# Performance work log

Measured on AMD Instinct MI355X. Metric: run time of the kernel, lower is better.

## Reference

```python
import jax, jax.numpy as jnp
import numpy as np

K = 3
PAD = 1
DIL = 1
BN_EPS = 1e-5


def _unfold(x, k, pad, dil):
    # torch F.unfold with stride=1: (bs, c, h, w) -> (bs, c*k*k, h*w), c slowest.
    bs, c, h, w = x.shape
    xp = jnp.pad(x, ((0, 0), (0, 0), (pad, pad), (pad, pad)))
    cols = [xp[:, :, i * dil:i * dil + h, j * dil:j * dil + w]
            for i in range(k) for j in range(k)]
    return jnp.stack(cols, axis=2).reshape(bs, c * k * k, h * w)


def setup_inputs() -> dict:
    key = jax.random.key(0)
    ks = jax.random.split(key, 4)
    bs, c, h, w = 8, 3, 512, 512
    kk = K * K
    kernel = jax.random.normal(ks[0], (bs, kk, h, w), jnp.float32)
    inp = jax.random.normal(ks[1], (bs, c, h, w), jnp.float32)
    inp0 = jax.random.normal(ks[2], (bs, c, h, w), jnp.float32)
    conv_w = jax.random.normal(ks[3], (kk, kk * 3, 3, 3), jnp.float32) * 0.05
    return {
        "kernel": kernel,
        "input": inp,
        "input0": inp0,
        "conv_w": conv_w,
        "bn_gamma": jnp.ones((kk,), jnp.float32),
        "bn_beta": jnp.zeros((kk,), jnp.float32),
        "bn_mean": jnp.zeros((kk,), jnp.float32),
        "bn_var": jnp.ones((kk,), jnp.float32),
    }


def reference(kernel, input, input0, conv_w, bn_gamma, bn_beta, bn_mean, bn_var):
    bs, c, h, w = input.shape
    kk = K * K
    mid = (kk - 1) // 2  # 4 for K=3
    # im2col: (bs, c*k*k, h*w) = (bs, 27, hw)
    im = _unfold(input, K, PAD, DIL)
    # overwrite 3 center rows with input0
    im = im.at[:, mid:mid + 3, :].set(input0.reshape(bs, c, h * w))
    x = im.reshape(bs, c * kk, h, w)
    # 3x3 conv, 27 -> 9 channels, pad 1, no bias
    y = jax.lax.conv_general_dilated(
        x, conv_w, window_strides=(1, 1), padding=[(1, 1), (1, 1)],
        dimension_numbers=("NCHW", "OIHW", "NCHW"))
    # BatchNorm (inference: running stats)
    scale = (bn_gamma / jnp.sqrt(bn_var + BN_EPS))[None, :, None, None]
    shift = (bn_beta - bn_mean * bn_gamma / jnp.sqrt(bn_var + BN_EPS))[None, :, None, None]
    y = y * scale + shift
    # elementwise weighted reduce over the k*k axis
    out = jnp.einsum("bkp,bkp->bp", y.reshape(bs, kk, h * w),
                     kernel.reshape(bs, kk, h * w))
    return out.reshape(bs, 1, h, w)
```

## Files before the change

### kernel.cpp

```cpp
#include <hip/hip_runtime.h>

#define HW 512
#define CH 3
#define KK 9
#define BS 8
#define TW 32
#define TH 8


__global__ __launch_bounds__(256) void prep_kernel(
    const float* __restrict__ conv_w, const float* __restrict__ gamma,
    const float* __restrict__ beta, const float* __restrict__ mean,
    const float* __restrict__ var, float* __restrict__ ws) {
  const int tid = threadIdx.x;
  for (int t = tid; t < 675; t += 256) {
    int o = t % 9, tap = t / 9;
    int c = tap / 25, r = tap % 25, ey = r / 5, ex = r % 5;
    float s = gamma[o] * rsqrtf(var[o] + 1e-5f);
    float sum = 0.f;
    for (int dy = 0; dy < 3; ++dy) {
      int oy = ey - dy; if (oy < 0 || oy > 2) continue;
      for (int dx = 0; dx < 3; ++dx) {
        int ox = ex - dx; if (ox < 0 || ox > 2) continue;
        int off = oy * 3 + ox;
        if (c == 0 && off >= 4 && off <= 6) continue;
        sum += conv_w[((o * 27 + c * 9 + off) * 3 + dy) * 3 + dx];
      }
    }
    ws[t] = s * sum;
  }
  for (int t = tid; t < 243; t += 256) {
    int o = t % 9, tap = t / 9;
    int c = tap / 9, r = tap % 9, dy = r / 3, dx = r % 3;
    float s = gamma[o] * rsqrtf(var[o] + 1e-5f);
    ws[675 + t] = s * conv_w[((o * 27 + 4 + c) * 3 + dy) * 3 + dx];
  }
  for (int o = tid; o < 9; o += 256) {
    float s = gamma[o] * rsqrtf(var[o] + 1e-5f);
    ws[918 + o] = beta[o] - mean[o] * s;
  }
  for (int t = tid; t < 2187; t += 256) {
    int o = t % 9, q = t / 9;
    int ic = q / 9, r = q % 9, dy = r / 3, dx = r % 3;
    float s = gamma[o] * rsqrtf(var[o] + 1e-5f);
    ws[927 + t] = s * conv_w[((o * 27 + ic) * 3 + dy) * 3 + dx];
  }
}

__global__ __launch_bounds__(256) void main_kernel(
    const float* __restrict__ kern, const float* __restrict__ input,
    const float* __restrict__ input0, const float* __restrict__ ws,
    float* __restrict__ out) {
  __shared__ float in_t[3][TH + 4][TW + 4];
  __shared__ float in0_t[3][TH + 2][TW + 2];
  const int tid = threadIdx.x;
  const int b = blockIdx.z;
  const int x0 = blockIdx.x * TW, y0 = blockIdx.y * TH;
  const float* inp_b = input + (long)b * CH * HW * HW;
  const float* inp0_b = input0 + (long)b * CH * HW * HW;

  float* lin = &in_t[0][0][0];
  for (int i = tid; i < 3 * (TH + 4) * (TW + 4); i += 256) {
    int c = i / ((TH + 4) * (TW + 4));
    int r = i % ((TH + 4) * (TW + 4));
    int ry = r / (TW + 4), rx = r % (TW + 4);
    int gy = y0 + ry - 2, gx = x0 + rx - 2;
    float v = 0.f;
    if ((unsigned)gy < HW && (unsigned)gx < HW) v = inp_b[(c * HW + gy) * HW + gx];
    lin[i] = v;
  }
  float* lin0 = &in0_t[0][0][0];
  for (int i = tid; i < 3 * (TH + 2) * (TW + 2); i += 256) {
    int c = i / ((TH + 2) * (TW + 2));
    int r = i % ((TH + 2) * (TW + 2));
    int ry = r / (TW + 2), rx = r % (TW + 2);
    int gy = y0 + ry - 1, gx = x0 + rx - 1;
    float v = 0.f;
    if ((unsigned)gy < HW && (unsigned)gx < HW) v = inp0_b[(c * HW + gy) * HW + gx];
    lin0[i] = v;
  }
  __syncthreads();

  const int tx = tid & 31, ty = tid >> 5;
  const int X = x0 + tx, Y = y0 + ty;
  float acc[9];
#pragma unroll
  for (int o = 0; o < 9; ++o) acc[o] = 0.f;

#pragma unroll
  for (int c = 0; c < 3; ++c)
#pragma unroll
    for (int ey = 0; ey < 5; ++ey)
#pragma unroll
      for (int ex = 0; ex < 5; ++ex) {
        float v = in_t[c][ty + ey][tx + ex];
        const float* w = ws + (c * 25 + ey * 5 + ex) * 9;
#pragma unroll
        for (int o = 0; o < 9; ++o) acc[o] = fmaf(w[o], v, acc[o]);
      }

#pragma unroll
  for (int c = 0; c < 3; ++c)
#pragma unroll
    for (int ey = 0; ey < 3; ++ey)
#pragma unroll
      for (int ex = 0; ex < 3; ++ex) {
        float v = in0_t[c][ty + ey][tx + ex];
        const float* w = ws + 675 + (c * 9 + ey * 3 + ex) * 9;
#pragma unroll
        for (int o = 0; o < 9; ++o) acc[o] = fmaf(w[o], v, acc[o]);
      }

  const float* kb = kern + (long)b * KK * (HW * HW) + Y * HW + X;
  float result = 0.f;
#pragma unroll
  for (int o = 0; o < 9; ++o)
    result = fmaf(kb[(long)o * (HW * HW)], acc[o] + ws[918 + o], result);
  out[((long)b * HW + Y) * HW + X] = result;
}

__global__ __launch_bounds__(256) void border_kernel(
    const float* __restrict__ kern, const float* __restrict__ input,
    const float* __restrict__ input0, const float* __restrict__ ws,
    float* __restrict__ out) {
  const int per_img = 4 * HW - 4;
  int idx = blockIdx.x * blockDim.x + threadIdx.x;
  if (idx >= BS * per_img) return;
  int b = idx / per_img, p = idx % per_img;
  int X, Y;
  if (p < HW) { Y = 0; X = p; }
  else if (p < 2 * HW) { Y = HW - 1; X = p - HW; }
  else if (p < 3 * HW - 2) { X = 0; Y = p - 2 * HW + 1; }
  else { X = HW - 1; Y = p - (3 * HW - 2) + 1; }

  const float* inp_b = input + (long)b * CH * HW * HW;
  const float* inp0_b = input0 + (long)b * CH * HW * HW;
  float acc[9];
#pragma unroll
  for (int o = 0; o < 9; ++o) acc[o] = 0.f;

  for (int dy = 0; dy < 3; ++dy) {
    int yy = Y + dy - 1;
    if ((unsigned)yy >= HW) continue;
    for (int dx = 0; dx < 3; ++dx) {
      int xx = X + dx - 1;
      if ((unsigned)xx >= HW) continue;
      for (int c = 0; c < 3; ++c)
        for (int oy = 0; oy < 3; ++oy) {
          int iy = yy + oy - 1;
          for (int ox = 0; ox < 3; ++ox) {
            int off = oy * 3 + ox;
            if (c == 0 && off >= 4 && off <= 6) continue;
            int ix = xx + ox - 1;
            float v = 0.f;
            if ((unsigned)iy < HW && (unsigned)ix < HW)
              v = inp_b[(c * HW + iy) * HW + ix];
            const float* w = ws + 927 + ((c * 9 + off) * 9 + dy * 3 + dx) * 9;
#pragma unroll
            for (int o = 0; o < 9; ++o) acc[o] = fmaf(w[o], v, acc[o]);
          }
        }
      for (int c = 0; c < 3; ++c) {
        float v = inp0_b[(c * HW + yy) * HW + xx];
        const float* w = ws + 675 + (c * 9 + dy * 3 + dx) * 9;
#pragma unroll
        for (int o = 0; o < 9; ++o) acc[o] = fmaf(w[o], v, acc[o]);
      }
    }
  }
  const float* kb = kern + (long)b * KK * (HW * HW) + Y * HW + X;
  float result = 0.f;
#pragma unroll
  for (int o = 0; o < 9; ++o)
    result = fmaf(kb[(long)o * (HW * HW)], acc[o] + ws[918 + o], result);
  out[((long)b * HW + Y) * HW + X] = result;
}

extern "C" void kernel_launch(void* const* d_in, const int* in_sizes, int n_in,
                              void* d_out, int out_size, void* d_ws, size_t ws_size,
                              hipStream_t stream) {
  const float* kern   = (const float*)d_in[0];
  const float* input  = (const float*)d_in[1];
  const float* input0 = (const float*)d_in[2];
  const float* conv_w = (const float*)d_in[3];
  const float* gamma  = (const float*)d_in[4];
  const float* beta   = (const float*)d_in[5];
  const float* mean   = (const float*)d_in[6];
  const float* var    = (const float*)d_in[7];
  float* out = (float*)d_out;
  float* ws  = (float*)d_ws;

  hipLaunchKernelGGL(prep_kernel, dim3(1), dim3(256), 0, stream,
                     conv_w, gamma, beta, mean, var, ws);
  dim3 grid(HW / TW, HW / TH, BS);
  hipLaunchKernelGGL(main_kernel, grid, dim3(256), 0, stream,
                     kern, input, input0, ws, out);
  int nb = (BS * (4 * HW - 4) + 255) / 256;
  hipLaunchKernelGGL(border_kernel, dim3(nb), dim3(256), 0, stream,
                     kern, input, input0, ws, out);
}
```

Before: 248.2 us.

## Compute four output pixels per thread with float4 LDS window loads

Enlarges the tile to 64x16 and has each thread produce four adjacent outputs. It reuses an 8-wide register window loaded with two float4 LDS reads per row, so each weight load feeds four FMAs. The workspace weights are realigned with padded rows so each row group starts on an aligned offset, and the kernel tensor and output are accessed with float4. The rolled c/ey loops and 36 accumulators raise register pressure and may lower occupancy, and the larger tile adds halo loads.

```diff
diff --git a/kernel.cpp b/kernel.cpp
--- a/kernel.cpp
+++ b/kernel.cpp
@@ -4,8 +4,8 @@
 #define CH 3
 #define KK 9
 #define BS 8
-#define TW 32
-#define TH 8
+#define TW 64
+#define TH 16
 
 
 __global__ __launch_bounds__(256) void prep_kernel(
@@ -27,23 +27,25 @@
         sum += conv_w[((o * 27 + c * 9 + off) * 3 + dy) * 3 + dx];
       }
     }
-    ws[t] = s * sum;
+    ws[(c * 5 + ey) * 48 + ex * 9 + o] = s * sum;
   }
   for (int t = tid; t < 243; t += 256) {
     int o = t % 9, tap = t / 9;
-    int c = tap / 9, r = tap % 9, dy = r / 3, dx = r % 3;
-    float s = gamma[o] * rsqrtf(var[o] + 1e-5f);
-    ws[675 + t] = s * conv_w[((o * 27 + 4 + c) * 3 + dy) * 3 + dx];
+    int c = tap / 9, r = tap % 9;
+    float s = gamma[o] * rsqrtf(var[o] + 1e-5f);
+    int ey = r / 3, ex = r % 3;
+    ws[720 + c * 96 + r * 9 + o] =
+        s * conv_w[((o * 27 + 4 + c) * 3 + ey) * 3 + ex];
   }
   for (int o = tid; o < 9; o += 256) {
     float s = gamma[o] * rsqrtf(var[o] + 1e-5f);
-    ws[918 + o] = beta[o] - mean[o] * s;
+    ws[1008 + o] = beta[o] - mean[o] * s;
   }
   for (int t = tid; t < 2187; t += 256) {
     int o = t % 9, q = t / 9;
     int ic = q / 9, r = q % 9, dy = r / 3, dx = r % 3;
     float s = gamma[o] * rsqrtf(var[o] + 1e-5f);
-    ws[927 + t] = s * conv_w[((o * 27 + ic) * 3 + dy) * 3 + dx];
+    ws[1024 + t] = s * conv_w[((o * 27 + ic) * 3 + dy) * 3 + dx];
   }
 }
 
@@ -51,8 +53,8 @@
     const float* __restrict__ kern, const float* __restrict__ input,
     const float* __restrict__ input0, const float* __restrict__ ws,
     float* __restrict__ out) {
-  __shared__ float in_t[3][TH + 4][TW + 4];
-  __shared__ float in0_t[3][TH + 2][TW + 2];
+  __shared__ __align__(16) float in_t[3][TH + 4][TW + 4];
+  __shared__ __align__(16) float in0_t[3][TH + 2][TW + 4];
   const int tid = threadIdx.x;
   const int b = blockIdx.z;
   const int x0 = blockIdx.x * TW, y0 = blockIdx.y * TH;
@@ -70,10 +72,10 @@
     lin[i] = v;
   }
   float* lin0 = &in0_t[0][0][0];
-  for (int i = tid; i < 3 * (TH + 2) * (TW + 2); i += 256) {
-    int c = i / ((TH + 2) * (TW + 2));
-    int r = i % ((TH + 2) * (TW + 2));
-    int ry = r / (TW + 2), rx = r % (TW + 2);
+  for (int i = tid; i < 3 * (TH + 2) * (TW + 4); i += 256) {
+    int c = i / ((TH + 2) * (TW + 4));
+    int r = i % ((TH + 2) * (TW + 4));
+    int ry = r / (TW + 4), rx = r % (TW + 4);
     int gy = y0 + ry - 1, gx = x0 + rx - 1;
     float v = 0.f;
     if ((unsigned)gy < HW && (unsigned)gx < HW) v = inp0_b[(c * HW + gy) * HW + gx];
@@ -81,42 +83,70 @@
   }
   __syncthreads();
 
-  const int tx = tid & 31, ty = tid >> 5;
-  const int X = x0 + tx, Y = y0 + ty;
-  float acc[9];
-#pragma unroll
-  for (int o = 0; o < 9; ++o) acc[o] = 0.f;
-
-#pragma unroll
-  for (int c = 0; c < 3; ++c)
-#pragma unroll
-    for (int ey = 0; ey < 5; ++ey)
-#pragma unroll
-      for (int ex = 0; ex < 5; ++ex) {
-        float v = in_t[c][ty + ey][tx + ex];
-        const float* w = ws + (c * 25 + ey * 5 + ex) * 9;
-#pragma unroll
-        for (int o = 0; o < 9; ++o) acc[o] = fmaf(w[o], v, acc[o]);
-      }
-
-#pragma unroll
-  for (int c = 0; c < 3; ++c)
-#pragma unroll
-    for (int ey = 0; ey < 3; ++ey)
-#pragma unroll
-      for (int ex = 0; ex < 3; ++ex) {
-        float v = in0_t[c][ty + ey][tx + ex];
-        const float* w = ws + 675 + (c * 9 + ey * 3 + ex) * 9;
-#pragma unroll
-        for (int o = 0; o < 9; ++o) acc[o] = fmaf(w[o], v, acc[o]);
-      }
-
-  const float* kb = kern + (long)b * KK * (HW * HW) + Y * HW + X;
-  float result = 0.f;
+  const int tx = tid & 15, ty = tid >> 4;
+  const int bx = tx * 4;
+  const int Y = y0 + ty;
+
+  float acc[9][4];
 #pragma unroll
   for (int o = 0; o < 9; ++o)
-    result = fmaf(kb[(long)o * (HW * HW)], acc[o] + ws[918 + o], result);
-  out[((long)b * HW + Y) * HW + X] = result;
+#pragma unroll
+    for (int p = 0; p < 4; ++p) acc[o][p] = 0.f;
+
+#pragma unroll 1
+  for (int c = 0; c < 3; ++c) {
+#pragma unroll 1
+    for (int ey = 0; ey < 5; ++ey) {
+      const float4 lo = *(const float4*)(&in_t[c][ty + ey][bx]);
+      const float4 hi = *(const float4*)(&in_t[c][ty + ey][bx + 4]);
+      const float win[8] = {lo.x, lo.y, lo.z, lo.w, hi.x, hi.y, hi.z, hi.w};
+      const float* wg = ws + (c * 5 + ey) * 48;
+#pragma unroll
+      for (int ex = 0; ex < 5; ++ex)
+#pragma unroll
+        for (int o = 0; o < 9; ++o) {
+          const float w = wg[ex * 9 + o];
+#pragma unroll
+          for (int p = 0; p < 4; ++p)
+            acc[o][p] = fmaf(w, win[ex + p], acc[o][p]);
+        }
+    }
+  }
+
+#pragma unroll 1
+  for (int c = 0; c < 3; ++c) {
+#pragma unroll 1
+    for (int ey = 0; ey < 3; ++ey) {
+      const float4 lo = *(const float4*)(&in0_t[c][ty + ey][bx]);
+      const float4 hi = *(const float4*)(&in0_t[c][ty + ey][bx + 4]);
+      const float win[8] = {lo.x, lo.y, lo.z, lo.w, hi.x, hi.y, hi.z, hi.w};
+      const float* wg = ws + 720 + c * 96 + ey * 27;
+#pragma unroll
+      for (int ex = 0; ex < 3; ++ex)
+#pragma unroll
+        for (int o = 0; o < 9; ++o) {
+          const float w = wg[ex * 9 + o];
+#pragma unroll
+          for (int p = 0; p < 4; ++p)
+            acc[o][p] = fmaf(w, win[ex + p], acc[o][p]);
+        }
+    }
+  }
+
+  const long hw2 = (long)HW * HW;
+  const float* kb = kern + (long)b * KK * hw2 + (long)Y * HW + (x0 + bx);
+  float res0 = 0.f, res1 = 0.f, res2 = 0.f, res3 = 0.f;
+#pragma unroll
+  for (int o = 0; o < 9; ++o) {
+    const float sh = ws[1008 + o];
+    const float4 k4 = *(const float4*)(kb + (long)o * hw2);
+    res0 = fmaf(k4.x, acc[o][0] + sh, res0);
+    res1 = fmaf(k4.y, acc[o][1] + sh, res1);
+    res2 = fmaf(k4.z, acc[o][2] + sh, res2);
+    res3 = fmaf(k4.w, acc[o][3] + sh, res3);
+  }
+  *(float4*)(out + ((long)b * HW + Y) * HW + (x0 + bx)) =
+      make_float4(res0, res1, res2, res3);
 }
 
 __global__ __launch_bounds__(256) void border_kernel(
@@ -155,14 +185,14 @@
             float v = 0.f;
             if ((unsigned)iy < HW && (unsigned)ix < HW)
               v = inp_b[(c * HW + iy) * HW + ix];
-            const float* w = ws + 927 + ((c * 9 + off) * 9 + dy * 3 + dx) * 9;
+            const float* w = ws + 1024 + ((c * 9 + off) * 9 + dy * 3 + dx) * 9;
 #pragma unroll
             for (int o = 0; o < 9; ++o) acc[o] = fmaf(w[o], v, acc[o]);
           }
         }
       for (int c = 0; c < 3; ++c) {
         float v = inp0_b[(c * HW + yy) * HW + xx];
-        const float* w = ws + 675 + (c * 9 + dy * 3 + dx) * 9;
+        const float* w = ws + 720 + c * 96 + (dy * 3 + dx) * 9;
 #pragma unroll
         for (int o = 0; o < 9; ++o) acc[o] = fmaf(w[o], v, acc[o]);
       }
@@ -172,7 +202,7 @@
   float result = 0.f;
 #pragma unroll
   for (int o = 0; o < 9; ++o)
-    result = fmaf(kb[(long)o * (HW * HW)], acc[o] + ws[918 + o], result);
+    result = fmaf(kb[(long)o * (HW * HW)], acc[o] + ws[1008 + o], result);
   out[((long)b * HW + Y) * HW + X] = result;
 }
 
```

After: 241.7 us. -2.6%, faster.
